# Performance work log

Hardware: AMD Instinct MI355X
Metric: run time of the kernel (lower is better)

The kernel has to match this reference:

```python
import jax, jax.numpy as jnp
import numpy as np

B, S, DIM = 2, 2048, 4096
NH, NKV, HD = 32, 8, 128          # head_dim = dim // n_heads
BLOCK = 16                         # paged-cache block size
NBLK_PER_SEQ = S // BLOCK          # 128
NUM_BLOCKS = B * NBLK_PER_SEQ      # 256 physical blocks
SCALE = 1.0 / np.sqrt(HD).astype(np.float32)


def _rope(x, fc):
    # x: [B,S,H,HD]; fc: [S,1,HD//2,2] (cos,sin) -- matches apply_rotary_emb
    xr = x.astype(jnp.float32).reshape(*x.shape[:-1], HD // 2, 2)
    cos, sin = fc[..., 0], fc[..., 1]
    out = jnp.stack([xr[..., 0] * cos - xr[..., 1] * sin,
                     xr[..., 1] * cos + xr[..., 0] * sin], axis=-1)
    return out.reshape(x.shape).astype(x.dtype)


def setup_inputs() -> dict:
    key = jax.random.key(0)
    ks = jax.random.split(key, 3)
    x = jax.random.normal(ks[0], (B, S, DIM), jnp.float32)
    wqkv_w = jax.random.normal(ks[1], ((NH + 2 * NKV) * HD, DIM), jnp.float32) * (DIM ** -0.5)
    wo_w = jax.random.normal(ks[2], (DIM, DIM), jnp.float32) * (DIM ** -0.5)
    # rotary table: [S, 1, HD/2, 2] so it broadcasts over (B, S, H, HD/2)
    pos = jnp.arange(S, dtype=jnp.float32)
    inv = 10000.0 ** (-jnp.arange(0, HD, 2, dtype=jnp.float32) / HD)
    ang = pos[:, None] * inv[None, :]
    freqs_cis = jnp.stack([jnp.cos(ang), jnp.sin(ang)], -1)[:, None, :, :]
    k_cache = jnp.zeros((NUM_BLOCKS, BLOCK, NKV, HD), jnp.float32)
    v_cache = jnp.zeros((NUM_BLOCKS, BLOCK, NKV, HD), jnp.float32)
    block_table = jnp.arange(B * NBLK_PER_SEQ, dtype=jnp.int32).reshape(B, NBLK_PER_SEQ)
    seqlens_k = jnp.full((B,), S, jnp.int32)
    return {"x": x, "wqkv_w": wqkv_w, "wo_w": wo_w, "freqs_cis": freqs_cis,
            "k_cache": k_cache, "v_cache": v_cache,
            "block_table": block_table, "seqlens_k": seqlens_k}


def reference(x, wqkv_w, wo_w, freqs_cis, k_cache, v_cache, block_table, seqlens_k):
    # fused QKV projection
    qkv = x @ wqkv_w.T                                   # [B,S,(NH+2*NKV)*HD]
    q, k, v = jnp.split(qkv, [NH * HD, (NH + NKV) * HD], axis=-1)
    q = q.reshape(B, S, NH, HD)
    k = k.reshape(B, S, NKV, HD)
    v = v.reshape(B, S, NKV, HD)
    q = _rope(q, freqs_cis)
    k = _rope(k, freqs_cis)
    # paged KV-cache write (prefill): slot = block_table[b, t//BLOCK]*BLOCK + t%BLOCK
    t = jnp.arange(S)
    slots = block_table[:, t // BLOCK] * BLOCK + (t % BLOCK)[None, :]    # [B,S]
    flat = slots.reshape(-1)
    kc = k_cache.reshape(NUM_BLOCKS * BLOCK, NKV, HD).at[flat].set(k.reshape(B * S, NKV, HD))
    vc = v_cache.reshape(NUM_BLOCKS * BLOCK, NKV, HD).at[flat].set(v.reshape(B * S, NKV, HD))
    # block-table indexed attention: gather K/V back through the page table
    kk = kc[slots]                                       # [B,S,NKV,HD]
    vv = vc[slots]                                       # [B,S,NKV,HD]
    G = NH // NKV                                        # GQA group size
    qg = q.reshape(B, S, NKV, G, HD)
    scores = jnp.einsum('bqkgd,bskd->bkgqs', qg, kk) * SCALE  # [B,NKV,G,S,S]
    qpos = jnp.arange(S)[:, None]
    kpos = jnp.arange(S)[None, :]
    causal = kpos <= qpos                                # [S,S]
    valid = kpos[None] < seqlens_k[:, None, None]        # [B,S,S]
    mask = (causal[None] & valid)[:, None, None]         # [B,1,1,S,S]
    scores = jnp.where(mask, scores, -jnp.inf)
    p = jax.nn.softmax(scores, axis=-1)
    attn = jnp.einsum('bkgqs,bskd->bqkgd', p, vv).reshape(B, S, NH * HD)
    return attn @ wo_w.T
```

## Files before the change

### kernel.cpp

```cpp
#include <hip/hip_runtime.h>
#include <hip/hip_fp16.h>

typedef _Float16 f16;
typedef _Float16 f16x4 __attribute__((ext_vector_type(4)));
typedef _Float16 f16x8 __attribute__((ext_vector_type(8)));
typedef float    f32x4 __attribute__((ext_vector_type(4)));

#define NEG_INF (-__builtin_inff())
#define AS1 __attribute__((address_space(1)))
#define AS3 __attribute__((address_space(3)))
#define GLOAD_LDS16(g, l) \
    __builtin_amdgcn_global_load_lds((AS1 const void*)(g), (AS3 void*)(l), 16, 0, 0)

__global__ __launch_bounds__(256) void cvt_f32_f16(const float* __restrict__ in,
                                                   f16* __restrict__ out, int n4) {
    int i = blockIdx.x * 256 + threadIdx.x;
    if (i >= n4) return;
    float4 v = ((const float4*)in)[i];
    f16x4 h = {(f16)v.x, (f16)v.y, (f16)v.z, (f16)v.w};
    ((f16x4*)out)[i] = h;
}

template <typename CT>
__global__ __launch_bounds__(256) void gemm_bt(const f16* __restrict__ A,
                                               const f16* __restrict__ Bt,
                                               CT* __restrict__ C, int M, int N, int K) {
    __shared__ f16 As[128 * 32];
    __shared__ f16 Bs[128 * 32];
    const int tid  = threadIdx.x;
    const int wave = tid >> 6, lane = tid & 63;
    const int quad = lane >> 4, m16 = lane & 15;
    const int waveM = (wave >> 1) * 64, waveN = (wave & 1) * 64;
    const int bm = blockIdx.y * 128, bn = blockIdx.x * 128;

    f32x4 acc[4][4];
#pragma unroll
    for (int i = 0; i < 4; ++i)
#pragma unroll
        for (int j = 0; j < 4; ++j)
#pragma unroll
            for (int e = 0; e < 4; ++e) acc[i][j][e] = 0.f;

    const f16* gA[2]; const f16* gB[2]; f16* lA[2]; f16* lB[2];
#pragma unroll
    for (int it = 0; it < 2; ++it) {
        int slot = wave * 128 + it * 64 + lane;
        int row  = slot >> 2;
        int c    = (slot - (row >> 1)) & 3;
        gA[it] = A  + (size_t)(bm + row) * K + c * 8;
        gB[it] = Bt + (size_t)(bn + row) * K + c * 8;
        lA[it] = As + (size_t)(wave * 128 + it * 64) * 8;
        lB[it] = Bs + (size_t)(wave * 128 + it * 64) * 8;
    }
    const f16* apf[4]; const f16* bpf[4];
#pragma unroll
    for (int t = 0; t < 4; ++t) {
        int rowA = waveM + t * 16 + m16;
        int rowB = waveN + t * 16 + m16;
        apf[t] = As + rowA * 32 + (((quad + (rowA >> 1)) & 3) * 8);
        bpf[t] = Bs + rowB * 32 + (((quad + (rowB >> 1)) & 3) * 8);
    }

    for (int k0 = 0; k0 < K; k0 += 32) {
        __syncthreads();
#pragma unroll
        for (int it = 0; it < 2; ++it) {
            GLOAD_LDS16(gA[it] + k0, lA[it]);
            GLOAD_LDS16(gB[it] + k0, lB[it]);
        }
        __syncthreads();
        f16x8 af[4], bf[4];
#pragma unroll
        for (int t = 0; t < 4; ++t) af[t] = *(const f16x8*)apf[t];
#pragma unroll
        for (int t = 0; t < 4; ++t) bf[t] = *(const f16x8*)bpf[t];
#pragma unroll
        for (int i = 0; i < 4; ++i)
#pragma unroll
            for (int j = 0; j < 4; ++j)
                acc[i][j] = __builtin_amdgcn_mfma_f32_16x16x32_f16(af[i], bf[j], acc[i][j], 0, 0, 0);
    }

#pragma unroll
    for (int i = 0; i < 4; ++i)
#pragma unroll
        for (int r = 0; r < 4; ++r) {
            int row = bm + waveM + i * 16 + quad * 4 + r;
#pragma unroll
            for (int j = 0; j < 4; ++j) {
                int col = bn + waveN + j * 16 + m16;
                C[(size_t)row * N + col] = (CT)acc[i][j][r];
            }
        }
}

__global__ __launch_bounds__(256) void rope_qk(const f16* __restrict__ qkv,
                                               const float* __restrict__ freqs,
                                               f16* __restrict__ qh,
                                               f16* __restrict__ kk) {
    int idx  = blockIdx.x * 256 + threadIdx.x;
    int row  = idx / 2560;
    int p    = idx - row * 2560;
    int b    = row >> 11, s = row & 2047;
    int head = p >> 6, i = p & 63;
    const f16* src = qkv + (size_t)row * 6144 + head * 128 + 2 * i;
    float v0 = (float)src[0], v1 = (float)src[1];
    float c  = freqs[s * 128 + 2 * i];
    float sn = freqs[s * 128 + 2 * i + 1];
    float r0 = v0 * c - v1 * sn;
    float r1 = v1 * c + v0 * sn;
    f16* dst = (head < 32)
        ? qh + (((size_t)(b * 32 + head)) * 2048 + s) * 128 + 2 * i
        : kk + (((size_t)(b * 8 + head - 32)) * 2048 + s) * 128 + 2 * i;
    dst[0] = (f16)r0; dst[1] = (f16)r1;
}

__global__ __launch_bounds__(256) void transpose_v(const f16* __restrict__ qkv,
                                                   f16* __restrict__ vvt) {
    __shared__ f16 T[64][72];
    const int st = blockIdx.x, dt = blockIdx.y;
    const int b = blockIdx.z >> 3, kvh = blockIdx.z & 7;
    const int tid = threadIdx.x;
    const int sr = tid >> 3, c8 = (tid & 7) * 8;
#pragma unroll
    for (int rep = 0; rep < 2; ++rep) {
        int sl = rep * 32 + sr;
        *(f16x8*)&T[sl][c8] =
            *(const f16x8*)(qkv + (size_t)(b * 2048 + st * 64 + sl) * 6144
                            + 5120 + kvh * 128 + dt * 64 + c8);
    }
    __syncthreads();
#pragma unroll
    for (int rep = 0; rep < 2; ++rep) {
        int dl = rep * 32 + sr;
        f16x8 v;
#pragma unroll
        for (int j = 0; j < 8; ++j) v[j] = T[c8 + j][dl];
        *(f16x8*)(vvt + (((size_t)(b * 8 + kvh)) * 128 + dt * 64 + dl) * 2048
                  + st * 64 + c8) = v;
    }
}

__global__ __launch_bounds__(256) void attn_fused(const f16* __restrict__ qh,
                                                  const f16* __restrict__ kk,
                                                  const f16* __restrict__ vvt,
                                                  const int* __restrict__ seqlens,
                                                  f16* __restrict__ out) {
    __shared__ f16 KsPs[64 * 136];
    __shared__ f16 Vs[128][72];
    const int pair = blockIdx.x;
    const int h = blockIdx.y, b = blockIdx.z;
    const int kvh = h >> 2;
    const int tid = threadIdx.x, wave = tid >> 6, lane = tid & 63;
    const int quad = lane >> 4, m16 = lane & 15;
    f16* Ps = KsPs;

    const int seqlen = seqlens[b];
    const f16* kbp = kk  + ((size_t)(b * 8 + kvh) * 2048) * 128;
    const f16* vbp = vvt + ((size_t)(b * 8 + kvh) * 128) * 2048;

    for (int half = 0; half < 2; ++half) {
        const int qt = half ? pair : (31 - pair);
        const int qbase = qt * 64;
        const int qw = qbase + wave * 16;

        const f16* qptr = qh + (((size_t)(b * 32 + h)) * 2048 + qw + m16) * 128;
        f16x8 qf[4];
#pragma unroll
        for (int c = 0; c < 4; ++c) qf[c] = *(const f16x8*)(qptr + c * 32 + quad * 8);

        float m_i[4], l_i[4];
        f32x4 oacc[8];
#pragma unroll
        for (int r = 0; r < 4; ++r) { m_i[r] = NEG_INF; l_i[r] = 0.f; }
#pragma unroll
        for (int dt = 0; dt < 8; ++dt)
#pragma unroll
            for (int e = 0; e < 4; ++e) oacc[dt][e] = 0.f;

        int kmax = qbase + 64; if (seqlen < kmax) kmax = seqlen;

        for (int kt = 0; kt < kmax; kt += 64) {
            __syncthreads();
#pragma unroll
            for (int it = 0; it < 4; ++it) {
                int g = it * 256 + tid;
                int r_ = g >> 4, c8 = (g & 15) * 8;
                *(f16x8*)&KsPs[r_ * 136 + c8] = *(const f16x8*)(kbp + (size_t)(kt + r_) * 128 + c8);
            }
#pragma unroll
            for (int it = 0; it < 4; ++it) {
                int g = it * 256 + tid;
                int r_ = g >> 3, c8 = (g & 7) * 8;
                *(f16x8*)&Vs[r_][c8] = *(const f16x8*)(vbp + (size_t)r_ * 2048 + kt + c8);
            }
            __syncthreads();

            f32x4 sc[4];
#pragma unroll
            for (int nt = 0; nt < 4; ++nt) {
                f32x4 s = {0.f, 0.f, 0.f, 0.f};
#pragma unroll
                for (int c = 0; c < 4; ++c) {
                    f16x8 kf = *(const f16x8*)&KsPs[(nt * 16 + m16) * 136 + c * 32 + quad * 8];
                    s = __builtin_amdgcn_mfma_f32_16x16x32_f16(qf[c], kf, s, 0, 0, 0);
                }
                sc[nt] = s;
            }

            float sv[4][4];
            float mt[4] = {NEG_INF, NEG_INF, NEG_INF, NEG_INF};
#pragma unroll
            for (int nt = 0; nt < 4; ++nt) {
                int kpos = kt + nt * 16 + m16;
#pragma unroll
                for (int r = 0; r < 4; ++r) {
                    int qpos = qw + quad * 4 + r;
                    float sx = sc[nt][r] * 0.08838834764831845f;
                    sx = (kpos <= qpos && kpos < seqlen) ? sx : NEG_INF;
                    sv[nt][r] = sx;
                    mt[r] = fmaxf(mt[r], sx);
                }
            }
#pragma unroll
            for (int off = 1; off < 16; off <<= 1)
#pragma unroll
                for (int r = 0; r < 4; ++r)
                    mt[r] = fmaxf(mt[r], __shfl_xor(mt[r], off, 64));

            float alpha[4], mm[4];
#pragma unroll
            for (int r = 0; r < 4; ++r) {
                float mo = m_i[r];
                float mn = fmaxf(mo, mt[r]);
                float mmr = fmaxf(mn, -1e30f);
                alpha[r] = __expf(mo - mmr);
                m_i[r] = mn;
                mm[r] = mmr;
            }
            float rs[4] = {0.f, 0.f, 0.f, 0.f};
#pragma unroll
            for (int nt = 0; nt < 4; ++nt)
#pragma unroll
                for (int r = 0; r < 4; ++r) {
                    float pv = __expf(sv[nt][r] - mm[r]);
                    sv[nt][r] = pv;
                    rs[r] += pv;
                }
#pragma unroll
            for (int off = 1; off < 16; off <<= 1)
#pragma unroll
                for (int r = 0; r < 4; ++r) rs[r] += __shfl_xor(rs[r], off, 64);
#pragma unroll
            for (int r = 0; r < 4; ++r) l_i[r] = l_i[r] * alpha[r] + rs[r];
#pragma unroll
            for (int dt = 0; dt < 8; ++dt)
#pragma unroll
                for (int r = 0; r < 4; ++r) oacc[dt][r] *= alpha[r];

            __syncthreads();

#pragma unroll
            for (int nt = 0; nt < 4; ++nt)
#pragma unroll
                for (int r = 0; r < 4; ++r)
                    Ps[(wave * 16 + quad * 4 + r) * 72 + nt * 16 + m16] = (f16)sv[nt][r];

            f16x8 pf[2];
#pragma unroll
            for (int c = 0; c < 2; ++c)
                pf[c] = *(const f16x8*)&Ps[(wave * 16 + m16) * 72 + c * 32 + quad * 8];
#pragma unroll
            for (int dt = 0; dt < 8; ++dt)
#pragma unroll
                for (int c = 0; c < 2; ++c) {
                    f16x8 vf = *(const f16x8*)&Vs[dt * 16 + m16][c * 32 + quad * 8];
                    oacc[dt] = __builtin_amdgcn_mfma_f32_16x16x32_f16(pf[c], vf, oacc[dt], 0, 0, 0);
                }
        }

#pragma unroll
        for (int r = 0; r < 4; ++r) {
            int qpos = qw + quad * 4 + r;
            float inv = 1.0f / l_i[r];
            f16* op = out + ((size_t)b * 2048 + qpos) * 4096 + h * 128;
#pragma unroll
            for (int dt = 0; dt < 8; ++dt)
                op[dt * 16 + m16] = (f16)(oacc[dt][r] * inv);
        }
    }
}

extern "C" void kernel_launch(void* const* d_in, const int* in_sizes, int n_in,
                              void* d_out, int out_size, void* d_ws, size_t ws_size,
                              hipStream_t stream) {
    const float* x     = (const float*)d_in[0];
    const float* wqkv  = (const float*)d_in[1];
    const float* wo    = (const float*)d_in[2];
    const float* freqs = (const float*)d_in[3];
    const int*   seql  = (const int*)d_in[7];
    float* out = (float*)d_out;

    char* ws = (char*)d_ws;
    size_t o = 0;
    f16* xh    = (f16*)(ws + o); o += (size_t)4096 * 4096 * 2;
    f16* wqkvh = (f16*)(ws + o); o += (size_t)6144 * 4096 * 2;
    f16* woh   = (f16*)(ws + o); o += (size_t)4096 * 4096 * 2;
    f16* qkvh  = (f16*)(ws + o); o += (size_t)4096 * 6144 * 2;
    f16* qhp   = (f16*)(ws + o); o += (size_t)4096 * 4096 * 2;
    f16* kkp   = (f16*)(ws + o); o += (size_t)4096 * 8 * 128 * 2;
    f16* vvt   = (f16*)(ws + o); o += (size_t)4096 * 8 * 128 * 2;
    f16* attnh = xh;

    cvt_f32_f16<<<16384, 256, 0, stream>>>(x, xh, 4194304);
    cvt_f32_f16<<<24576, 256, 0, stream>>>(wqkv, wqkvh, 6291456);
    cvt_f32_f16<<<16384, 256, 0, stream>>>(wo, woh, 4194304);

    gemm_bt<f16><<<dim3(48, 32), 256, 0, stream>>>(xh, wqkvh, qkvh, 4096, 6144, 4096);

    rope_qk<<<40960, 256, 0, stream>>>(qkvh, freqs, qhp, kkp);
    transpose_v<<<dim3(32, 2, 16), 256, 0, stream>>>(qkvh, vvt);

    attn_fused<<<dim3(16, 32, 2), 256, 0, stream>>>(qhp, kkp, vvt, seql, attnh);

    gemm_bt<float><<<dim3(32, 32), 256, 0, stream>>>(attnh, woh, out, 4096, 4096, 4096);
}
```

Before: 947.0 us.

## Replace GEMM with 256x256-tile double-buffered kernel using XCD-aware block swizzle

Both projection GEMMs switch from a 128x128-tile, single-buffered, fully synchronised kernel to a 512-thread 256x256-tile kernel with K-step 64. The new kernel double-buffers LDS, staggers direct global-to-LDS loads across four MFMA phases with explicit waitcnt and barriers, raises wave priority around the MFMA blocks, and remaps block IDs so tiles are grouped per XCD. The goal is more reuse per loaded byte, and hiding global load latency behind matrix math. In exchange it uses 128KB of LDS and many more accumulator registers, which limits occupancy to one workgroup per CU and makes correctness depend on hand-placed waitcnt counts.

```diff
diff --git a/kernel.cpp b/kernel.cpp
--- a/kernel.cpp
+++ b/kernel.cpp
@@ -11,6 +11,9 @@
 #define AS3 __attribute__((address_space(3)))
 #define GLOAD_LDS16(g, l) \
     __builtin_amdgcn_global_load_lds((AS1 const void*)(g), (AS3 void*)(l), 16, 0, 0)
+#define BARRIER() do { asm volatile("" ::: "memory"); \
+                       __builtin_amdgcn_s_barrier(); \
+                       asm volatile("" ::: "memory"); } while (0)
 
 __global__ __launch_bounds__(256) void cvt_f32_f16(const float* __restrict__ in,
                                                    f16* __restrict__ out, int n4) {
@@ -22,75 +25,161 @@
 }
 
 template <typename CT>
-__global__ __launch_bounds__(256) void gemm_bt(const f16* __restrict__ A,
+__global__ __launch_bounds__(512) void gemm256(const f16* __restrict__ A,
                                                const f16* __restrict__ Bt,
-                                               CT* __restrict__ C, int M, int N, int K) {
-    __shared__ f16 As[128 * 32];
-    __shared__ f16 Bs[128 * 32];
+                                               CT* __restrict__ C,
+                                               int M, int N, int K) {
+    __shared__ __align__(16) f16 smem[65536];
+    f16* LA = smem;
+    f16* LB = smem + 32768;
+
     const int tid  = threadIdx.x;
     const int wave = tid >> 6, lane = tid & 63;
     const int quad = lane >> 4, m16 = lane & 15;
-    const int waveM = (wave >> 1) * 64, waveN = (wave & 1) * 64;
-    const int bm = blockIdx.y * 128, bn = blockIdx.x * 128;
-
-    f32x4 acc[4][4];
-#pragma unroll
-    for (int i = 0; i < 4; ++i)
+    const int wm = wave >> 2, wn = wave & 3;
+
+    const int ntn = N >> 8;
+    const int nwg = (M >> 8) * ntn;
+    const int q8 = nwg >> 3, r8 = nwg & 7;
+    const int xcd = blockIdx.x & 7, idx = blockIdx.x >> 3;
+    const int swz = (xcd < r8 ? xcd * (q8 + 1) : r8 * (q8 + 1) + (xcd - r8) * q8) + idx;
+    const int bm = (swz / ntn) << 8;
+    const int bn = (swz % ntn) << 8;
+
+    const int rowW = tid >> 3;
+    const int gsrc = (tid & 7) ^ (rowW & 7);
+    const f16* gA0 = A  + (size_t)(bm + rowW) * K + gsrc * 8;
+    const f16* gA1 = A  + (size_t)(bm + 128 + rowW) * K + gsrc * 8;
+    const f16* gB0 = Bt + (size_t)(bn + rowW) * K + gsrc * 8;
+    const f16* gB1 = Bt + (size_t)(bn + 128 + rowW) * K + gsrc * 8;
+    const size_t rstep = (size_t)64 * K;
+    const int lw = wave * 512;
+
+#define STG(dstbase, gp, kt) do { \
+    GLOAD_LDS16((gp) + (size_t)(kt) * 64,         (dstbase) + lw); \
+    GLOAD_LDS16((gp) + (size_t)(kt) * 64 + rstep, (dstbase) + lw + 4096); } while (0)
+
+    int foff[2];
+#pragma unroll
+    for (int ks = 0; ks < 2; ++ks)
+        foff[ks] = (((ks << 2) | quad) ^ (m16 & 7)) * 8;
+    const int arow = wm * 8192 + m16 * 64;
+    const int brow = (wn >> 1) * 8192 + (wn & 1) * 4096 + m16 * 64;
+
+    f32x4 acc[8][4];
+#pragma unroll
+    for (int i = 0; i < 8; ++i)
 #pragma unroll
         for (int j = 0; j < 4; ++j)
 #pragma unroll
             for (int e = 0; e < 4; ++e) acc[i][j][e] = 0.f;
 
-    const f16* gA[2]; const f16* gB[2]; f16* lA[2]; f16* lB[2];
-#pragma unroll
-    for (int it = 0; it < 2; ++it) {
-        int slot = wave * 128 + it * 64 + lane;
-        int row  = slot >> 2;
-        int c    = (slot - (row >> 1)) & 3;
-        gA[it] = A  + (size_t)(bm + row) * K + c * 8;
-        gB[it] = Bt + (size_t)(bn + row) * K + c * 8;
-        lA[it] = As + (size_t)(wave * 128 + it * 64) * 8;
-        lB[it] = Bs + (size_t)(wave * 128 + it * 64) * 8;
+    const int NT = K >> 6;
+
+    STG(LA, gA0, 0); STG(LA + 8192, gA1, 0);
+    STG(LB, gB0, 0); STG(LB + 8192, gB1, 0);
+    STG(LB + 16384, gB0, 1); STG(LB + 16384 + 8192, gB1, 1);
+    asm volatile("s_waitcnt vmcnt(4)" ::: "memory");
+    BARRIER();
+
+    f16x8 af[4][2], bf0[2][2], bf1[2][2];
+
+    for (int t = 0; t < NT; ++t) {
+        const int bo = (t & 1) * 16384;
+        const f16* pa = LA + bo + arow;
+        const f16* pb = LB + bo + brow;
+
+#pragma unroll
+        for (int mt = 0; mt < 4; ++mt)
+#pragma unroll
+            for (int ks = 0; ks < 2; ++ks)
+                af[mt][ks] = *(const f16x8*)(pa + mt * 1024 + foff[ks]);
+#pragma unroll
+        for (int nt = 0; nt < 2; ++nt)
+#pragma unroll
+            for (int ks = 0; ks < 2; ++ks)
+                bf0[nt][ks] = *(const f16x8*)(pb + nt * 1024 + foff[ks]);
+        if (t + 1 < NT) STG(LA + (bo ^ 16384), gA0, t + 1);
+        BARRIER();
+        asm volatile("s_waitcnt lgkmcnt(0)" ::: "memory");
+        __builtin_amdgcn_s_setprio(1);
+#pragma unroll
+        for (int mt = 0; mt < 4; ++mt)
+#pragma unroll
+            for (int nt = 0; nt < 2; ++nt)
+#pragma unroll
+                for (int ks = 0; ks < 2; ++ks)
+                    acc[mt][nt] = __builtin_amdgcn_mfma_f32_16x16x32_f16(
+                        af[mt][ks], bf0[nt][ks], acc[mt][nt], 0, 0, 0);
+        __builtin_amdgcn_s_setprio(0);
+        BARRIER();
+
+#pragma unroll
+        for (int nt = 0; nt < 2; ++nt)
+#pragma unroll
+            for (int ks = 0; ks < 2; ++ks)
+                bf1[nt][ks] = *(const f16x8*)(pb + (nt + 2) * 1024 + foff[ks]);
+        if (t + 1 < NT) STG(LA + (bo ^ 16384) + 8192, gA1, t + 1);
+        BARRIER();
+        asm volatile("s_waitcnt lgkmcnt(0)" ::: "memory");
+        __builtin_amdgcn_s_setprio(1);
+#pragma unroll
+        for (int mt = 0; mt < 4; ++mt)
+#pragma unroll
+            for (int nt = 0; nt < 2; ++nt)
+#pragma unroll
+                for (int ks = 0; ks < 2; ++ks)
+                    acc[mt][nt + 2] = __builtin_amdgcn_mfma_f32_16x16x32_f16(
+                        af[mt][ks], bf1[nt][ks], acc[mt][nt + 2], 0, 0, 0);
+        __builtin_amdgcn_s_setprio(0);
+        BARRIER();
+
+#pragma unroll
+        for (int mt = 0; mt < 4; ++mt)
+#pragma unroll
+            for (int ks = 0; ks < 2; ++ks)
+                af[mt][ks] = *(const f16x8*)(pa + (mt + 4) * 1024 + foff[ks]);
+        if (t + 2 < NT) STG(LB + bo, gB0, t + 2);
+        BARRIER();
+        asm volatile("s_waitcnt lgkmcnt(0)" ::: "memory");
+        __builtin_amdgcn_s_setprio(1);
+#pragma unroll
+        for (int mt = 0; mt < 4; ++mt)
+#pragma unroll
+            for (int nt = 0; nt < 2; ++nt)
+#pragma unroll
+                for (int ks = 0; ks < 2; ++ks)
+                    acc[mt + 4][nt + 2] = __builtin_amdgcn_mfma_f32_16x16x32_f16(
+                        af[mt][ks], bf1[nt][ks], acc[mt + 4][nt + 2], 0, 0, 0);
+        __builtin_amdgcn_s_setprio(0);
+        BARRIER();
+
+        if (t + 2 < NT) STG(LB + bo + 8192, gB1, t + 2);
+        BARRIER();
+        __builtin_amdgcn_s_setprio(1);
+#pragma unroll
+        for (int mt = 0; mt < 4; ++mt)
+#pragma unroll
+            for (int nt = 0; nt < 2; ++nt)
+#pragma unroll
+                for (int ks = 0; ks < 2; ++ks)
+                    acc[mt + 4][nt] = __builtin_amdgcn_mfma_f32_16x16x32_f16(
+                        af[mt][ks], bf0[nt][ks], acc[mt + 4][nt], 0, 0, 0);
+        __builtin_amdgcn_s_setprio(0);
+        if (t + 2 < NT) { asm volatile("s_waitcnt vmcnt(4)" ::: "memory"); }
+        else            { asm volatile("s_waitcnt vmcnt(0)" ::: "memory"); }
+        BARRIER();
     }
-    const f16* apf[4]; const f16* bpf[4];
-#pragma unroll
-    for (int t = 0; t < 4; ++t) {
-        int rowA = waveM + t * 16 + m16;
-        int rowB = waveN + t * 16 + m16;
-        apf[t] = As + rowA * 32 + (((quad + (rowA >> 1)) & 3) * 8);
-        bpf[t] = Bs + rowB * 32 + (((quad + (rowB >> 1)) & 3) * 8);
-    }
-
-    for (int k0 = 0; k0 < K; k0 += 32) {
-        __syncthreads();
-#pragma unroll
-        for (int it = 0; it < 2; ++it) {
-            GLOAD_LDS16(gA[it] + k0, lA[it]);
-            GLOAD_LDS16(gB[it] + k0, lB[it]);
-        }
-        __syncthreads();
-        f16x8 af[4], bf[4];
-#pragma unroll
-        for (int t = 0; t < 4; ++t) af[t] = *(const f16x8*)apf[t];
-#pragma unroll
-        for (int t = 0; t < 4; ++t) bf[t] = *(const f16x8*)bpf[t];
-#pragma unroll
-        for (int i = 0; i < 4; ++i)
-#pragma unroll
-            for (int j = 0; j < 4; ++j)
-                acc[i][j] = __builtin_amdgcn_mfma_f32_16x16x32_f16(af[i], bf[j], acc[i][j], 0, 0, 0);
-    }
-
-#pragma unroll
-    for (int i = 0; i < 4; ++i)
+#undef STG
+
+#pragma unroll
+    for (int mt = 0; mt < 8; ++mt)
 #pragma unroll
         for (int r = 0; r < 4; ++r) {
-            int row = bm + waveM + i * 16 + quad * 4 + r;
-#pragma unroll
-            for (int j = 0; j < 4; ++j) {
-                int col = bn + waveN + j * 16 + m16;
-                C[(size_t)row * N + col] = (CT)acc[i][j][r];
-            }
+            int row = bm + wm * 128 + mt * 16 + quad * 4 + r;
+            CT* cp = C + (size_t)row * N + bn + wn * 64 + m16;
+#pragma unroll
+            for (int nt = 0; nt < 4; ++nt) cp[nt * 16] = (CT)acc[mt][nt][r];
         }
 }
 
@@ -316,12 +405,12 @@
     cvt_f32_f16<<<24576, 256, 0, stream>>>(wqkv, wqkvh, 6291456);
     cvt_f32_f16<<<16384, 256, 0, stream>>>(wo, woh, 4194304);
 
-    gemm_bt<f16><<<dim3(48, 32), 256, 0, stream>>>(xh, wqkvh, qkvh, 4096, 6144, 4096);
+    gemm256<f16><<<384, 512, 0, stream>>>(xh, wqkvh, qkvh, 4096, 6144, 4096);
 
     rope_qk<<<40960, 256, 0, stream>>>(qkvh, freqs, qhp, kkp);
     transpose_v<<<dim3(32, 2, 16), 256, 0, stream>>>(qkvh, vvt);
 
     attn_fused<<<dim3(16, 32, 2), 256, 0, stream>>>(qhp, kkp, vvt, seql, attnh);
 
-    gemm_bt<float><<<dim3(32, 32), 256, 0, stream>>>(attnh, woh, out, 4096, 4096, 4096);
-}
+    gemm256<float><<<256, 512, 0, stream>>>(attnh, woh, out, 4096, 4096, 4096);
+}
```

Result: faster. 842.3 us (-11.1%).
